# Kernel tuning notes

Hardware: AMD Instinct MI355X
Metric: run time of the kernel (lower is better)

The kernel has to match this reference:

```python
import jax, jax.numpy as jnp
import numpy as np

B, C, N, K = 2, 128, 10000, 16


def setup_inputs() -> dict:
    key = jax.random.key(0)
    k1, k2, k3, k4 = jax.random.split(key, 4)
    x = jax.random.normal(k1, (B, C, N, 1), dtype=jnp.float32)
    edge_index = jax.random.randint(k2, (2, B, N, K), 0, N, dtype=jnp.int32)
    W = jax.random.normal(k3, (C, C), dtype=jnp.float32) * 0.05  # 1x1 conv C->C, no bias
    a = jax.random.normal(k4, (2 * C,), dtype=jnp.float32) * 0.05  # 1x1 conv 2C->1, no bias
    return {"x": x, "edge_index": edge_index, "W": W, "a": a}


def reference(x, edge_index, W, a):
    # x: [B,C,N,1], edge_index: [2,B,N,K]
    b, c, n, _ = x.shape
    k = edge_index.shape[-1]
    xs = x[..., 0]  # [B,C,N]
    wh = jnp.einsum('oc,bcn->bon', W, xs)  # 1x1 conv W(x): [B,C,N]
    # batched_index_select: gather along node dim -> [B,C,N,K]
    idx_i = edge_index[1].reshape(b, 1, n * k)
    idx_j = edge_index[0].reshape(b, 1, n * k)
    whi = jnp.take_along_axis(wh, idx_i, axis=2).reshape(b, c, n, k)
    whj = jnp.take_along_axis(wh, idx_j, axis=2).reshape(b, c, n, k)
    # a(cat([whi, whj], dim=1)) with a: 2C->1 == a_i . whi + a_j . whj
    e = jnp.einsum('c,bcnk->bnk', a[:c], whi) + jnp.einsum('c,bcnk->bnk', a[c:], whj)
    e = jax.nn.leaky_relu(e, negative_slope=0.2)
    A = jax.nn.softmax(e, axis=-1)  # [B,N,K]; dropout omitted (eval mode)
    h = jnp.einsum('bcnk,bnk->bcn', whj, A)  # mul + sum over K
    return h[..., None]  # [B,C,N,1]
```

## Files before the change

kernel.cpp:

```cpp
#include <hip/hip_runtime.h>


#define BB 2
#define CC 128
#define NN 10000
#define KK 16
#define TNG 64
#define TNA 16

typedef unsigned int uint32;

__device__ __forceinline__ uint32 bf16pair(float lo, float hi) {
  uint32 ulo = __float_as_uint(lo);
  uint32 uhi = __float_as_uint(hi);
  ulo += 0x7fffu + ((ulo >> 16) & 1u);
  uhi += 0x7fffu + ((uhi >> 16) & 1u);
  return (ulo >> 16) | (uhi & 0xffff0000u);
}

__global__ __launch_bounds__(512) void gat_gemm(
    const float* __restrict__ x,
    const float* __restrict__ W,
    const float* __restrict__ a,
    uint32* __restrict__ wht,
    float* __restrict__ si,
    float* __restrict__ sj) {
  __shared__ float xs[CC][TNG];
  __shared__ float red[2][8][TNG];

  const int b    = blockIdx.y;
  const int n0   = blockIdx.x * TNG;
  const int t    = threadIdx.x;
  const int lane = t & 63;
  const int wv   = t >> 6;

  const float* xb = x + (size_t)b * CC * NN;
#pragma unroll
  for (int i = 0; i < 16; ++i) {
    int e = t + i * 512;
    int c = e >> 6, n = e & 63;
    int gn = n0 + n;
    xs[c][n] = (gn < NN) ? xb[c * NN + gn] : 0.f;
  }
  __syncthreads();

  const int co = __builtin_amdgcn_readfirstlane(wv << 4);
  const float4* Wv = (const float4*)(W + co * CC);

  float acc[16];
#pragma unroll
  for (int j = 0; j < 16; ++j) acc[j] = 0.f;

  for (int c0 = 0; c0 < CC; c0 += 8) {
    float xv[8];
#pragma unroll
    for (int u = 0; u < 8; ++u) xv[u] = xs[c0 + u][lane];
    const int q = c0 >> 2;
#pragma unroll
    for (int j = 0; j < 16; ++j) {
      float4 w0 = Wv[j * 32 + q];
      float4 w1 = Wv[j * 32 + q + 1];
      acc[j] = fmaf(w0.x, xv[0], acc[j]);
      acc[j] = fmaf(w0.y, xv[1], acc[j]);
      acc[j] = fmaf(w0.z, xv[2], acc[j]);
      acc[j] = fmaf(w0.w, xv[3], acc[j]);
      acc[j] = fmaf(w1.x, xv[4], acc[j]);
      acc[j] = fmaf(w1.y, xv[5], acc[j]);
      acc[j] = fmaf(w1.z, xv[6], acc[j]);
      acc[j] = fmaf(w1.w, xv[7], acc[j]);
    }
  }

  const float* ai = a + co;
  const float* aj = a + CC + co;
  float psi = 0.f, psj = 0.f;
#pragma unroll
  for (int j = 0; j < 16; ++j) {
    psi = fmaf(ai[j], acc[j], psi);
    psj = fmaf(aj[j], acc[j], psj);
  }
  red[0][wv][lane] = psi;
  red[1][wv][lane] = psj;

  const int gn = n0 + lane;
  if (gn < NN) {
    uint32 pk[8];
#pragma unroll
    for (int j = 0; j < 8; ++j) pk[j] = bf16pair(acc[2 * j], acc[2 * j + 1]);
    uint4* wb = (uint4*)(wht + ((size_t)(b * NN + gn)) * (CC / 2) + (co >> 1));
    wb[0] = make_uint4(pk[0], pk[1], pk[2], pk[3]);
    wb[1] = make_uint4(pk[4], pk[5], pk[6], pk[7]);
  }

  __syncthreads();
  if (t < TNG) {
    int g = n0 + t;
    if (g < NN) {
      float s1 = 0.f, s2 = 0.f;
#pragma unroll
      for (int w = 0; w < 8; ++w) { s1 += red[0][w][t]; s2 += red[1][w][t]; }
      si[b * NN + g] = s1;
      sj[b * NN + g] = s2;
    }
  }
}

__global__ __launch_bounds__(256) void gat_gather(
    const int* __restrict__ ei,
    const uint32* __restrict__ wht,
    const float* __restrict__ si,
    const float* __restrict__ sj,
    float* __restrict__ out) {
  __shared__ float Am[TNA][KK];
  __shared__ int   jd[TNA][KK];
  __shared__ float outT[CC][TNA + 1];

  const int b  = blockIdx.y;
  const int n0 = blockIdx.x * TNA;
  const int t  = threadIdx.x;

  const int* eij = ei + b * NN * KK;
  const int* eii = ei + (BB + b) * NN * KK;
  const float* sib = si + b * NN;
  const float* sjb = sj + b * NN;

  {
    int nn = t >> 4, k = t & 15, gn = n0 + nn;
    float el = 0.f; int jj = 0;
    if (gn < NN) {
      jj = eij[gn * KK + k];
      int ii = eii[gn * KK + k];
      float v = sib[ii] + sjb[jj];
      el = (v > 0.f) ? v : 0.2f * v;
    }
    Am[nn][k] = el;
    jd[nn][k] = jj;
  }
  __syncthreads();

  if (t < TNA) {
    float mx = Am[t][0];
#pragma unroll
    for (int k = 1; k < KK; ++k) mx = fmaxf(mx, Am[t][k]);
    float s = 0.f, ex[KK];
#pragma unroll
    for (int k = 0; k < KK; ++k) { ex[k] = __expf(Am[t][k] - mx); s += ex[k]; }
    float inv = 1.f / s;
#pragma unroll
    for (int k = 0; k < KK; ++k) Am[t][k] = ex[k] * inv;
  }
  __syncthreads();

  const int cp = t & 63;
  const int nw = t >> 6;
  const uint32* whtb = wht + (size_t)b * NN * (CC / 2);
  for (int nn = nw; nn < TNA; nn += 4) {
    int gn = n0 + nn;
    float ax = 0.f, ay = 0.f;
    if (gn < NN) {
      int idx[KK]; float wk[KK];
#pragma unroll
      for (int k = 0; k < KK; ++k) { idx[k] = jd[nn][k]; wk[k] = Am[nn][k]; }
      uint32 v[KK];
#pragma unroll
      for (int k = 0; k < KK; ++k)
        v[k] = whtb[(size_t)idx[k] * (CC / 2) + cp];
#pragma unroll
      for (int k = 0; k < KK; ++k) {
        ax = fmaf(wk[k], __uint_as_float(v[k] << 16), ax);
        ay = fmaf(wk[k], __uint_as_float(v[k] & 0xffff0000u), ay);
      }
    }
    outT[2 * cp][nn]     = ax;
    outT[2 * cp + 1][nn] = ay;
  }
  __syncthreads();

  float* outb = out + (size_t)b * CC * NN;
#pragma unroll
  for (int i = 0; i < (CC * TNA) / 256; ++i) {
    int e = t + i * 256;
    int c = e >> 4, nn = e & 15;
    int gn = n0 + nn;
    if (gn < NN) outb[c * NN + gn] = outT[c][nn];
  }
}

extern "C" void kernel_launch(void* const* d_in, const int* in_sizes, int n_in,
                              void* d_out, int out_size, void* d_ws, size_t ws_size,
                              hipStream_t stream) {
  const float* x  = (const float*)d_in[0];
  const int*   ei = (const int*)d_in[1];
  const float* W  = (const float*)d_in[2];
  const float* a  = (const float*)d_in[3];
  float* out = (float*)d_out;

  uint32* wht = (uint32*)d_ws;
  float*  si  = (float*)(wht + (size_t)BB * NN * (CC / 2));
  float*  sj  = si + BB * NN;

  dim3 g1((NN + TNG - 1) / TNG, BB);
  dim3 g2((NN + TNA - 1) / TNA, BB);
  gat_gemm<<<g1, 512, 0, stream>>>(x, W, a, wht, si, sj);
  gat_gather<<<g2, 256, 0, stream>>>(ei, wht, si, sj, out);
}
```

Before: 105.7 us.

## Use bf16 MFMA for projection GEMM and batch two nodes per gather iteration

The 1x1-conv GEMM now runs as bf16 MFMA 16x16x32 instructions. W and the x tile are converted to bf16 in padded LDS, replacing the scalar fp32 FMA loop that read W from global memory. The attention-score dot products now use cross-lane shuffle reductions, and block size drops to 256 threads. The gather kernel issues loads for two nodes at once using vectorised LDS reads, which increases memory-level parallelism. The trade-offs are reduced GEMM input precision (bf16 inputs instead of fp32) and more registers per thread in the gather.

```diff
diff --git a/kernel.cpp b/kernel.cpp
--- a/kernel.cpp
+++ b/kernel.cpp
@@ -7,8 +7,12 @@
 #define KK 16
 #define TNG 64
 #define TNA 16
+#define LSTR 136
 
 typedef unsigned int uint32;
+typedef unsigned short ushort16_t;
+typedef __attribute__((ext_vector_type(8))) short short8;
+typedef __attribute__((ext_vector_type(4))) float floatx4;
 
 __device__ __forceinline__ uint32 bf16pair(float lo, float hi) {
   uint32 ulo = __float_as_uint(lo);
@@ -18,89 +22,121 @@
   return (ulo >> 16) | (uhi & 0xffff0000u);
 }
 
-__global__ __launch_bounds__(512) void gat_gemm(
+__global__ __launch_bounds__(256) void gat_gemm(
     const float* __restrict__ x,
     const float* __restrict__ W,
     const float* __restrict__ a,
     uint32* __restrict__ wht,
     float* __restrict__ si,
     float* __restrict__ sj) {
-  __shared__ float xs[CC][TNG];
-  __shared__ float red[2][8][TNG];
-
-  const int b    = blockIdx.y;
-  const int n0   = blockIdx.x * TNG;
-  const int t    = threadIdx.x;
+  __shared__ ushort16_t Wl[CC * LSTR];
+  __shared__ ushort16_t xs[TNG * LSTR];
+  __shared__ float red[2][4][4][16];
+
+  const int b  = blockIdx.y;
+  const int n0 = blockIdx.x * TNG;
+  const int t  = threadIdx.x;
+
+  {
+    const float2* Wg = (const float2*)W;
+    uint32* Wd = (uint32*)Wl;
+#pragma unroll
+    for (int i = 0; i < 32; ++i) {
+      int f2 = t + i * 256;
+      float2 v = Wg[f2];
+      int o = f2 >> 6, c2 = f2 & 63;
+      Wd[o * 68 + c2] = bf16pair(v.x, v.y);
+    }
+  }
+  {
+    const float* xb = x + (size_t)b * CC * NN;
+    uint32* xd = (uint32*)xs;
+#pragma unroll
+    for (int i = 0; i < 16; ++i) {
+      int e = t + i * 256;
+      int n = e & 63, cp = e >> 6;
+      int c = cp * 2, gn = n0 + n;
+      float v0 = 0.f, v1 = 0.f;
+      if (gn < NN) { v0 = xb[c * NN + gn]; v1 = xb[(c + 1) * NN + gn]; }
+      xd[n * 68 + cp] = bf16pair(v0, v1);
+    }
+  }
+  __syncthreads();
+
+  const int w    = t >> 6;
   const int lane = t & 63;
-  const int wv   = t >> 6;
-
-  const float* xb = x + (size_t)b * CC * NN;
-#pragma unroll
-  for (int i = 0; i < 16; ++i) {
-    int e = t + i * 512;
-    int c = e >> 6, n = e & 63;
-    int gn = n0 + n;
-    xs[c][n] = (gn < NN) ? xb[c * NN + gn] : 0.f;
-  }
-  __syncthreads();
-
-  const int co = __builtin_amdgcn_readfirstlane(wv << 4);
-  const float4* Wv = (const float4*)(W + co * CC);
-
-  float acc[16];
-#pragma unroll
-  for (int j = 0; j < 16; ++j) acc[j] = 0.f;
-
-  for (int c0 = 0; c0 < CC; c0 += 8) {
-    float xv[8];
-#pragma unroll
-    for (int u = 0; u < 8; ++u) xv[u] = xs[c0 + u][lane];
-    const int q = c0 >> 2;
-#pragma unroll
-    for (int j = 0; j < 16; ++j) {
-      float4 w0 = Wv[j * 32 + q];
-      float4 w1 = Wv[j * 32 + q + 1];
-      acc[j] = fmaf(w0.x, xv[0], acc[j]);
-      acc[j] = fmaf(w0.y, xv[1], acc[j]);
-      acc[j] = fmaf(w0.z, xv[2], acc[j]);
-      acc[j] = fmaf(w0.w, xv[3], acc[j]);
-      acc[j] = fmaf(w1.x, xv[4], acc[j]);
-      acc[j] = fmaf(w1.y, xv[5], acc[j]);
-      acc[j] = fmaf(w1.z, xv[6], acc[j]);
-      acc[j] = fmaf(w1.w, xv[7], acc[j]);
-    }
-  }
-
-  const float* ai = a + co;
-  const float* aj = a + CC + co;
-  float psi = 0.f, psj = 0.f;
-#pragma unroll
-  for (int j = 0; j < 16; ++j) {
-    psi = fmaf(ai[j], acc[j], psi);
-    psj = fmaf(aj[j], acc[j], psj);
-  }
-  red[0][wv][lane] = psi;
-  red[1][wv][lane] = psj;
-
-  const int gn = n0 + lane;
-  if (gn < NN) {
-    uint32 pk[8];
-#pragma unroll
-    for (int j = 0; j < 8; ++j) pk[j] = bf16pair(acc[2 * j], acc[2 * j + 1]);
-    uint4* wb = (uint4*)(wht + ((size_t)(b * NN + gn)) * (CC / 2) + (co >> 1));
-    wb[0] = make_uint4(pk[0], pk[1], pk[2], pk[3]);
-    wb[1] = make_uint4(pk[4], pk[5], pk[6], pk[7]);
-  }
-
-  __syncthreads();
+  const int col  = lane & 15;
+  const int q    = lane >> 4;
+
+  floatx4 acc[2][4];
+#pragma unroll
+  for (int ci = 0; ci < 2; ++ci)
+#pragma unroll
+    for (int nj = 0; nj < 4; ++nj) acc[ci][nj] = (floatx4){0.f, 0.f, 0.f, 0.f};
+
+#pragma unroll
+  for (int s = 0; s < 4; ++s) {
+    const int ko = s * 32 + q * 8;
+    short8 af[2], bf[4];
+#pragma unroll
+    for (int ci = 0; ci < 2; ++ci)
+      af[ci] = *(const short8*)(Wl + (w * 32 + ci * 16 + col) * LSTR + ko);
+#pragma unroll
+    for (int nj = 0; nj < 4; ++nj)
+      bf[nj] = *(const short8*)(xs + (nj * 16 + col) * LSTR + ko);
+#pragma unroll
+    for (int ci = 0; ci < 2; ++ci)
+#pragma unroll
+      for (int nj = 0; nj < 4; ++nj)
+        acc[ci][nj] = __builtin_amdgcn_mfma_f32_16x16x32_bf16(af[ci], bf[nj], acc[ci][nj], 0, 0, 0);
+  }
+
+  float ar[2][4], aj4[2][4];
+#pragma unroll
+  for (int ci = 0; ci < 2; ++ci)
+#pragma unroll
+    for (int r = 0; r < 4; ++r) {
+      int ch = w * 32 + ci * 16 + q * 4 + r;
+      ar[ci][r]  = a[ch];
+      aj4[ci][r] = a[CC + ch];
+    }
+
+#pragma unroll
+  for (int nj = 0; nj < 4; ++nj) {
+    int node = n0 + nj * 16 + col;
+    float psi = 0.f, psj = 0.f;
+#pragma unroll
+    for (int ci = 0; ci < 2; ++ci) {
+#pragma unroll
+      for (int r = 0; r < 4; ++r) {
+        psi = fmaf(ar[ci][r], acc[ci][nj][r], psi);
+        psj = fmaf(aj4[ci][r], acc[ci][nj][r], psj);
+      }
+      if (node < NN) {
+        uint2 pk;
+        pk.x = bf16pair(acc[ci][nj][0], acc[ci][nj][1]);
+        pk.y = bf16pair(acc[ci][nj][2], acc[ci][nj][3]);
+        uint2* dst = (uint2*)(wht + ((size_t)(b * NN + node)) * (CC / 2) + w * 16 + ci * 8 + q * 2);
+        *dst = pk;
+      }
+    }
+    psi += __shfl_down(psi, 32);
+    psi += __shfl_down(psi, 16);
+    psj += __shfl_down(psj, 32);
+    psj += __shfl_down(psj, 16);
+    if (q == 0) { red[0][w][nj][col] = psi; red[1][w][nj][col] = psj; }
+  }
+  __syncthreads();
+
   if (t < TNG) {
-    int g = n0 + t;
-    if (g < NN) {
+    int gn = n0 + t;
+    if (gn < NN) {
+      int nj = t >> 4, cl = t & 15;
       float s1 = 0.f, s2 = 0.f;
 #pragma unroll
-      for (int w = 0; w < 8; ++w) { s1 += red[0][w][t]; s2 += red[1][w][t]; }
-      si[b * NN + g] = s1;
-      sj[b * NN + g] = s2;
+      for (int ww = 0; ww < 4; ++ww) { s1 += red[0][ww][nj][cl]; s2 += red[1][ww][nj][cl]; }
+      si[b * NN + gn] = s1;
+      sj[b * NN + gn] = s2;
     }
   }
 }
@@ -154,25 +190,43 @@
   const int cp = t & 63;
   const int nw = t >> 6;
   const uint32* whtb = wht + (size_t)b * NN * (CC / 2);
-  for (int nn = nw; nn < TNA; nn += 4) {
-    int gn = n0 + nn;
-    float ax = 0.f, ay = 0.f;
-    if (gn < NN) {
-      int idx[KK]; float wk[KK];
-#pragma unroll
-      for (int k = 0; k < KK; ++k) { idx[k] = jd[nn][k]; wk[k] = Am[nn][k]; }
-      uint32 v[KK];
+#pragma unroll
+  for (int half = 0; half < 2; ++half) {
+    int na = nw + half * 4;
+    int idx[2][KK]; float wk[2][KK];
+#pragma unroll
+    for (int p = 0; p < 2; ++p) {
+      int nn = na + p * 8;
+      const uint4*   jp = (const uint4*)&jd[nn][0];
+      const float4*  ap = (const float4*)&Am[nn][0];
+#pragma unroll
+      for (int g = 0; g < 4; ++g) {
+        uint4  jv = jp[g];
+        float4 av = ap[g];
+        idx[p][4 * g + 0] = jv.x; idx[p][4 * g + 1] = jv.y;
+        idx[p][4 * g + 2] = jv.z; idx[p][4 * g + 3] = jv.w;
+        wk[p][4 * g + 0] = av.x;  wk[p][4 * g + 1] = av.y;
+        wk[p][4 * g + 2] = av.z;  wk[p][4 * g + 3] = av.w;
+      }
+    }
+    uint32 v[2][KK];
+#pragma unroll
+    for (int p = 0; p < 2; ++p)
 #pragma unroll
       for (int k = 0; k < KK; ++k)
-        v[k] = whtb[(size_t)idx[k] * (CC / 2) + cp];
+        v[p][k] = whtb[(size_t)idx[p][k] * (CC / 2) + cp];
+#pragma unroll
+    for (int p = 0; p < 2; ++p) {
+      int nn = na + p * 8;
+      float ax = 0.f, ay = 0.f;
 #pragma unroll
       for (int k = 0; k < KK; ++k) {
-        ax = fmaf(wk[k], __uint_as_float(v[k] << 16), ax);
-        ay = fmaf(wk[k], __uint_as_float(v[k] & 0xffff0000u), ay);
-      }
-    }
-    outT[2 * cp][nn]     = ax;
-    outT[2 * cp + 1][nn] = ay;
+        ax = fmaf(wk[p][k], __uint_as_float(v[p][k] << 16), ax);
+        ay = fmaf(wk[p][k], __uint_as_float(v[p][k] & 0xffff0000u), ay);
+      }
+      outT[2 * cp][nn]     = ax;
+      outT[2 * cp + 1][nn] = ay;
+    }
   }
   __syncthreads();
 
@@ -201,6 +255,6 @@
 
   dim3 g1((NN + TNG - 1) / TNG, BB);
   dim3 g2((NN + TNA - 1) / TNA, BB);
-  gat_gemm<<<g1, 512, 0, stream>>>(x, W, a, wht, si, sj);
+  gat_gemm<<<g1, 256, 0, stream>>>(x, W, a, wht, si, sj);
   gat_gather<<<g2, 256, 0, stream>>>(ei, wht, si, sj, out);
 }
```

Measured after the change: 88.19 us. 16.5% less time.
